# Kernel optimization log

Measured on AMD Instinct MI355X. Metric: run time of the kernel, lower is better.

## Reference

```python
import jax, jax.numpy as jnp
import numpy as np

L_LAYERS = 6
D = 768
H = 12
DH = D // H
FF = 3072
B = 32
LX = 256
LY = 128
EPS = 1e-6
NEG = -1e9


def setup_inputs() -> dict:
    key = jax.random.key(0)
    ks = jax.random.split(key, 24)
    s = 0.02
    f32 = jnp.float32
    inp = {
        'y': jax.random.normal(ks[0], (B, LY, D), f32),
        'x': jax.random.normal(ks[1], (B, LX, D), f32),
        'y_mask': jnp.zeros((B, 1, 1, LY), bool),
        'x_mask': jnp.zeros((B, 1, 1, LX), bool),
        'y_pos': jnp.arange(B * LY, dtype=jnp.int32).reshape(B, LY),
        'bbox': jax.random.normal(ks[2], (B, LX, 4), f32),
        # encoder (SA) params, stacked over layers; attn weight order: q,k,v,merge
        'enc_attn_w': jax.random.normal(ks[3], (L_LAYERS, 4, D, D), f32) * s,
        'enc_attn_b': jnp.zeros((L_LAYERS, 4, D), f32),
        'enc_ffn_w1': jax.random.normal(ks[4], (L_LAYERS, D, FF), f32) * s,
        'enc_ffn_b1': jnp.zeros((L_LAYERS, FF), f32),
        'enc_ffn_w2': jax.random.normal(ks[5], (L_LAYERS, FF, D), f32) * s,
        'enc_ffn_b2': jnp.zeros((L_LAYERS, D), f32),
        'enc_ln_g': jnp.ones((L_LAYERS, 2, D), f32),
        'enc_ln_b': jnp.zeros((L_LAYERS, 2, D), f32),
        # decoder (RELAGA) params; two attentions per layer (self, cross)
        'dec_attn_w': jax.random.normal(ks[6], (L_LAYERS, 2, 4, D, D), f32) * s,
        'dec_attn_b': jnp.zeros((L_LAYERS, 2, 4, D), f32),
        'dec_ffn_w1': jax.random.normal(ks[7], (L_LAYERS, D, FF), f32) * s,
        'dec_ffn_b1': jnp.zeros((L_LAYERS, FF), f32),
        'dec_ffn_w2': jax.random.normal(ks[8], (L_LAYERS, FF, D), f32) * s,
        'dec_ffn_b2': jnp.zeros((L_LAYERS, D), f32),
        'dec_ln_g': jnp.ones((L_LAYERS, 3, D), f32),
        'dec_ln_b': jnp.zeros((L_LAYERS, 3, D), f32),
    }
    return inp


def _layernorm(t, g, b):
    m = jnp.mean(t, axis=-1, keepdims=True)
    v = jnp.mean((t - m) ** 2, axis=-1, keepdims=True)
    return g * (t - m) / jnp.sqrt(v + EPS) + b


def _heads(t, w, bias):
    # [B,L,D] -> [B,H,L,DH]
    nb = t.shape[0]
    return (t @ w + bias).reshape(nb, -1, H, DH).transpose(0, 2, 1, 3)


def _mha(v, k, q, mask, w, bias, rel=None):
    # w: [4,D,D] (q,k,v,merge), bias: [4,D]; rel: [B,1,Lq,Lq] or None
    qh = _heads(q, w[0], bias[0])
    kh = _heads(k, w[1], bias[1])
    vh = _heads(v, w[2], bias[2])
    scores = jnp.einsum('bhqd,bhkd->bhqk', qh, kh) / np.sqrt(DH).astype(np.float32)
    scores = jnp.where(mask, NEG, scores)
    att = jax.nn.softmax(scores, axis=-1)
    out = jnp.einsum('bhqk,bhkd->bhqd', att, vh)
    if rel is not None:
        out = jnp.einsum('bhqp,bhpd->bhqd', rel, out)  # bbox-relational matmul
    nb = q.shape[0]
    out = out.transpose(0, 2, 1, 3).reshape(nb, -1, D)
    return out @ w[3] + bias[3]


def _ffn(t, w1, b1, w2, b2):
    return jnp.maximum(t @ w1 + b1, 0.0) @ w2 + b2


def reference(y, x, y_mask, x_mask, y_pos, bbox,
              enc_attn_w, enc_attn_b, enc_ffn_w1, enc_ffn_b1, enc_ffn_w2, enc_ffn_b2,
              enc_ln_g, enc_ln_b,
              dec_attn_w, dec_attn_b, dec_ffn_w1, dec_ffn_b1, dec_ffn_w2, dec_ffn_b2,
              dec_ln_g, dec_ln_b):
    # bbox cosine-similarity relation matrix (softmax over last dim), shared across heads
    prod = jnp.einsum('bic,bjc->bij', bbox, bbox)
    n = jnp.sqrt(jnp.sum(bbox * bbox, axis=-1))          # [B,LX]
    denom = n[:, :, None] * n[:, None, :]                 # [B,LX,LX]
    sim = jax.nn.softmax(prod / denom, axis=2)[:, None]   # [B,1,LX,LX] broadcasts over heads

    for i in range(L_LAYERS):  # encoder: SA stack over y
        att = _mha(y, y, y, y_mask, enc_attn_w[i], enc_attn_b[i])
        y = _layernorm(y + att, enc_ln_g[i, 0], enc_ln_b[i, 0])
        f = _ffn(y, enc_ffn_w1[i], enc_ffn_b1[i], enc_ffn_w2[i], enc_ffn_b2[i])
        y = _layernorm(y + f, enc_ln_g[i, 1], enc_ln_b[i, 1])

    for i in range(L_LAYERS):  # decoder: RELAGA stack over x
        att = _mha(x, x, x, x_mask, dec_attn_w[i, 0], dec_attn_b[i, 0], rel=sim)
        x = _layernorm(x + att, dec_ln_g[i, 0], dec_ln_b[i, 0])
        att = _mha(y, y, x, y_mask, dec_attn_w[i, 1], dec_attn_b[i, 1], rel=sim)
        x = _layernorm(x + att, dec_ln_g[i, 1], dec_ln_b[i, 1])
        f = _ffn(x, dec_ffn_w1[i], dec_ffn_b1[i], dec_ffn_w2[i], dec_ffn_b2[i])
        x = _layernorm(x + f, dec_ln_g[i, 2], dec_ln_b[i, 2])

    return (y, x)
```

## Files before the change

kernel.cpp:

```cpp
#include <hip/hip_runtime.h>

#define DEV __device__ __forceinline__

constexpr int NB  = 32;
constexpr int LXc = 256;
constexpr int LYc = 128;
constexpr int Dc  = 768;
constexpr int NH  = 12;
constexpr int FFc = 3072;

typedef unsigned short u16;
typedef float f32x4 __attribute__((ext_vector_type(4)));
typedef short s16x8 __attribute__((ext_vector_type(8)));

DEV u16 f2bf(float f) {
  unsigned u = __float_as_uint(f);
  u += 0x7FFFu + ((u >> 16) & 1u);
  return (u16)(u >> 16);
}
DEV float bf2f(u16 w) { return __uint_as_float(((unsigned)w) << 16); }
DEV float ldf(const void* p, long long i, int isbf) {
  return isbf ? bf2f(((const u16*)p)[i]) : ((const float*)p)[i];
}

DEV void gload16(const void* g, void* l) {
  __builtin_amdgcn_global_load_lds(
      (const __attribute__((address_space(1))) void*)g,
      (__attribute__((address_space(3))) void*)l, 16, 0, 0);
}
DEV void barx() {
  asm volatile("" ::: "memory");
  __builtin_amdgcn_s_barrier();
  asm volatile("" ::: "memory");
}

__global__ void k_detect(const u16* y, int* flag) {
  if (threadIdx.x == 0) {
    int cnt = 0;
    for (int i = 0; i < 256; ++i) {
      u16 w = y[i];
      int e = (w >> 7) & 0xFF;
      if (e == 0 || (e >= 112 && e <= 140)) cnt++;
    }
    *flag = (cnt >= 200) ? 1 : 0;
  }
}

__global__ void k_ingest_b(const void* src, u16* dst, long long n, const int* flag) {
  int isbf = *flag;
  long long i = (long long)blockIdx.x * blockDim.x + threadIdx.x;
  long long st = (long long)gridDim.x * blockDim.x;
  for (; i < n; i += st) dst[i] = isbf ? ((const u16*)src)[i] : f2bf(((const float*)src)[i]);
}

__global__ void k_cvt(const void* src, float* dst, long long n, const int* flag) {
  int isbf = *flag;
  long long i = (long long)blockIdx.x * blockDim.x + threadIdx.x;
  long long st = (long long)gridDim.x * blockDim.x;
  for (; i < n; i += st) dst[i] = ldf(src, i, isbf);
}

__global__ void k_emit(const u16* ybuf, const u16* xbuf, void* out,
                       const int* flag, long long ny, long long nt) {
  int isbf = *flag;
  long long i = (long long)blockIdx.x * blockDim.x + threadIdx.x;
  long long st = (long long)gridDim.x * blockDim.x;
  for (; i < nt; i += st) {
    u16 v = (i < ny) ? ybuf[i] : xbuf[i - ny];
    if (isbf) ((u16*)out)[i] = v;
    else      ((float*)out)[i] = bf2f(v);
  }
}

__global__ __launch_bounds__(256) void k_wt(const void* src, u16* dst, int R, int C, const int* flag) {
  int isbf = *flag;
  __shared__ u16 t[32][33];
  long long base = (long long)blockIdx.z * R * C;
  int c0 = blockIdx.x * 32, r0 = blockIdx.y * 32;
  int tx = threadIdx.x & 31, ty = threadIdx.x >> 5;
#pragma unroll
  for (int k = 0; k < 4; ++k) {
    int r = r0 + ty + k * 8;
    t[ty + k * 8][tx] = f2bf(ldf(src, base + (long long)r * C + (c0 + tx), isbf));
  }
  __syncthreads();
#pragma unroll
  for (int k = 0; k < 4; ++k) {
    int c = c0 + ty + k * 8;
    dst[base + (long long)c * R + (r0 + tx)] = t[tx][ty + k * 8];
  }
}

__global__ __launch_bounds__(256) void k_bboxsim(const void* bbox, const int* flag, u16* sim) {
  int isbf = *flag;
  int b = blockIdx.x >> 8, i = blockIdx.x & 255;
  int j = threadIdx.x;
  long long base = (long long)b * LXc * 4;
  float a[4], c[4];
#pragma unroll
  for (int t = 0; t < 4; ++t) {
    a[t] = ldf(bbox, base + (long long)i * 4 + t, isbf);
    c[t] = ldf(bbox, base + (long long)j * 4 + t, isbf);
  }
  float dot = a[0]*c[0] + a[1]*c[1] + a[2]*c[2] + a[3]*c[3];
  float na  = sqrtf(a[0]*a[0] + a[1]*a[1] + a[2]*a[2] + a[3]*a[3]);
  float ncn = sqrtf(c[0]*c[0] + c[1]*c[1] + c[2]*c[2] + c[3]*c[3]);
  float v = dot / (na * ncn);
  __shared__ float r1[4], r2[4];
  float m = v;
  for (int o = 32; o; o >>= 1) m = fmaxf(m, __shfl_xor(m, o));
  if ((threadIdx.x & 63) == 0) r1[threadIdx.x >> 6] = m;
  __syncthreads();
  m = fmaxf(fmaxf(r1[0], r1[1]), fmaxf(r1[2], r1[3]));
  float e = __expf(v - m);
  float s = e;
  for (int o = 32; o; o >>= 1) s += __shfl_xor(s, o);
  if ((threadIdx.x & 63) == 0) r2[threadIdx.x >> 6] = s;
  __syncthreads();
  s = r2[0] + r2[1] + r2[2] + r2[3];
  sim[((long long)b * LXc + i) * LXc + j] = f2bf(e / s);
}

__global__ __launch_bounds__(256) void k_lnres3(u16* curb, const u16* delta,
                                                const void* g, long long gOff,
                                                const void* bb, long long bOff,
                                                const int* flag) {
  int isbf = *flag;
  long long row = blockIdx.x;
  u16* xr = curb + row * Dc;
  const u16* dr = delta + row * Dc;
  int t = threadIdx.x;
  float v[3];
  float s = 0.f;
#pragma unroll
  for (int i = 0; i < 3; ++i) { int c = t + i * 256; v[i] = bf2f(xr[c]) + bf2f(dr[c]); s += v[i]; }
  __shared__ float r1[4], r2[4];
  for (int o = 32; o; o >>= 1) s += __shfl_xor(s, o);
  if ((t & 63) == 0) r1[t >> 6] = s;
  __syncthreads();
  float mean = (r1[0] + r1[1] + r1[2] + r1[3]) * (1.0f / 768.0f);
  float s2 = 0.f;
#pragma unroll
  for (int i = 0; i < 3; ++i) { float d = v[i] - mean; s2 += d * d; }
  for (int o = 32; o; o >>= 1) s2 += __shfl_xor(s2, o);
  if ((t & 63) == 0) r2[t >> 6] = s2;
  __syncthreads();
  float var = (r2[0] + r2[1] + r2[2] + r2[3]) * (1.0f / 768.0f);
  float rstd = rsqrtf(var + 1e-6f);
#pragma unroll
  for (int i = 0; i < 3; ++i) {
    int c = t + i * 256;
    float o = ldf(g, gOff + c, isbf) * (v[i] - mean) * rstd + ldf(bb, bOff + c, isbf);
    xr[c] = f2bf(o);
  }
}

template<int DEC>
__global__ __launch_bounds__(256) void k_attn(const u16* __restrict__ Q,
                                              const u16* __restrict__ Kb,
                                              const u16* __restrict__ Vt,
                                              u16* __restrict__ Out,
                                              int Lq, int Lk) {
  __shared__ __align__(16) u16 Kl[64 * 64];
  __shared__ __align__(16) u16 Vl[64 * 64];
  __shared__ __align__(16) u16 Pl[4][16][72];
  const int tid = threadIdx.x, wid = tid >> 6, lane = tid & 63;
  const int qt = blockIdx.x, h = blockIdx.y, b = blockIdx.z;
  const int q0 = qt * 64 + wid * 16;
  const int rl = lane & 15, sx = lane >> 4;
  const int srow = lane >> 3;
  const int scol8 = ((lane & 7) ^ srow) << 3;

  s16x8 qa[2];
  {
    const u16* qrow = Q + ((long long)b * Lq + q0 + rl) * Dc + h * 64;
    qa[0] = *(const s16x8*)(qrow + sx * 8);
    qa[1] = *(const s16x8*)(qrow + 32 + sx * 8);
  }
  f32x4 o[4] = {};
  float m[4], l[4];
#pragma unroll
  for (int e = 0; e < 4; ++e) { m[e] = -3.0e38f; l[e] = 0.f; }

  const long long kbase = (long long)b * Lk * Dc + h * 64;
  const long long vbase = ((long long)b * Dc + h * 64) * Lk;

  for (int k0 = 0; k0 < Lk; k0 += 64) {
#pragma unroll
    for (int g = 0; g < 2; ++g) {
      int chunk = g * 4 + wid;
      gload16(Kb + kbase + (long long)(k0 + chunk * 8 + srow) * Dc + scol8,
              (char*)Kl + chunk * 1024);
    }
#pragma unroll
    for (int g = 0; g < 2; ++g) {
      int chunk = g * 4 + wid;
      gload16(Vt + vbase + (long long)(chunk * 8 + srow) * Lk + k0 + scol8,
              (char*)Vl + chunk * 1024);
    }
    asm volatile("s_waitcnt vmcnt(0)" ::: "memory");
    barx();

    f32x4 s[4];
#pragma unroll
    for (int n = 0; n < 4; ++n) {
      s16x8 b0 = *(const s16x8*)((char*)Kl + (n * 16 + rl) * 128 + ((sx    ) ^ (rl & 7)) * 16);
      s16x8 b1 = *(const s16x8*)((char*)Kl + (n * 16 + rl) * 128 + ((sx + 4) ^ (rl & 7)) * 16);
      f32x4 acc = {};
      acc = __builtin_amdgcn_mfma_f32_16x16x32_bf16(qa[0], b0, acc, 0, 0, 0);
      acc = __builtin_amdgcn_mfma_f32_16x16x32_bf16(qa[1], b1, acc, 0, 0, 0);
      s[n] = acc;
    }
#pragma unroll
    for (int n = 0; n < 4; ++n)
#pragma unroll
      for (int e = 0; e < 4; ++e) s[n][e] *= 0.125f;

#pragma unroll
    for (int e = 0; e < 4; ++e) {
      float v = fmaxf(fmaxf(s[0][e], s[1][e]), fmaxf(s[2][e], s[3][e]));
      v = fmaxf(v, __shfl_xor(v, 1));
      v = fmaxf(v, __shfl_xor(v, 2));
      v = fmaxf(v, __shfl_xor(v, 4));
      v = fmaxf(v, __shfl_xor(v, 8));
      float mn = fmaxf(m[e], v);
      float alpha = __expf(m[e] - mn);
      m[e] = mn;
      float ls = 0.f;
#pragma unroll
      for (int n = 0; n < 4; ++n) {
        float p = __expf(s[n][e] - mn);
        s[n][e] = p;
        ls += p;
      }
      ls += __shfl_xor(ls, 1);
      ls += __shfl_xor(ls, 2);
      ls += __shfl_xor(ls, 4);
      ls += __shfl_xor(ls, 8);
      l[e] = l[e] * alpha + ls;
#pragma unroll
      for (int n = 0; n < 4; ++n) o[n][e] *= alpha;
    }

#pragma unroll
    for (int e = 0; e < 4; ++e)
#pragma unroll
      for (int n = 0; n < 4; ++n)
        Pl[wid][sx * 4 + e][n * 16 + rl] = f2bf(s[n][e]);
    barx();

    s16x8 pa0 = *(const s16x8*)&Pl[wid][rl][sx * 8];
    s16x8 pa1 = *(const s16x8*)&Pl[wid][rl][32 + sx * 8];
#pragma unroll
    for (int n = 0; n < 4; ++n) {
      s16x8 v0 = *(const s16x8*)((char*)Vl + (n * 16 + rl) * 128 + ((sx    ) ^ (rl & 7)) * 16);
      s16x8 v1 = *(const s16x8*)((char*)Vl + (n * 16 + rl) * 128 + ((sx + 4) ^ (rl & 7)) * 16);
      o[n] = __builtin_amdgcn_mfma_f32_16x16x32_bf16(pa0, v0, o[n], 0, 0, 0);
      o[n] = __builtin_amdgcn_mfma_f32_16x16x32_bf16(pa1, v1, o[n], 0, 0, 0);
    }
    barx();
  }

#pragma unroll
  for (int e = 0; e < 4; ++e) l[e] = 1.0f / l[e];
  if (DEC) {
    u16* Op = Out + ((long long)b * Dc + h * 64) * LXc;
#pragma unroll
    for (int n = 0; n < 4; ++n) {
      union { u16 u[4]; uint2 d; } pk;
#pragma unroll
      for (int e = 0; e < 4; ++e) pk.u[e] = f2bf(o[n][e] * l[e]);
      *(uint2*)&Op[(long long)(n * 16 + rl) * LXc + q0 + sx * 4] = pk.d;
    }
  } else {
    u16* Op = Out + ((long long)b * Lq + q0) * Dc + h * 64;
#pragma unroll
    for (int n = 0; n < 4; ++n)
#pragma unroll
      for (int e = 0; e < 4; ++e)
        Op[(long long)(sx * 4 + e) * Dc + n * 16 + rl] = f2bf(o[n][e] * l[e]);
  }
}

struct G2 {
  const u16* A; long long lda, sAb, sAh;
  const u16* W; long long ldw, sWb, sWh;
  const float* bias; long long bOff;
  void* C; long long ldc, sCb, sCh;
  void* Ck; void* Cv; int vSeg;
  int Hdim; float scale; int relu; int Lseq;
};

template<int BM, int BN, int MODE>
__global__ __launch_bounds__(256, 2) void gemm2(G2 p, int M, int N, int K) {
  constexpr int BK = 64;
  __shared__ __align__(16) u16 Al[BM * BK];
  __shared__ __align__(16) u16 Bl[BN * BK];
  const int tid = threadIdx.x, wid = tid >> 6, lane = tid & 63;
  const int z = blockIdx.z, zb = z / p.Hdim, zh = z % p.Hdim;
  int bx = blockIdx.x, by = blockIdx.y;
  if (gridDim.z == 1) {
    int gx = gridDim.x, nwg = gx * gridDim.y;
    int orig = by * gx + bx;
    int q = nwg >> 3, r = nwg & 7, xcd = orig & 7, lin = orig >> 3;
    int wg = (xcd < r ? xcd * (q + 1) : r * (q + 1) + (xcd - r) * q) + lin;
    bx = wg % gx; by = wg / gx;
  }
  const u16* A = p.A + (long long)zb * p.sAb + (long long)zh * p.sAh;
  const u16* W = p.W + (long long)zb * p.sWb + (long long)zh * p.sWh;
  const int m0 = by * BM, n0 = bx * BN;
  const int wr = wid >> 1, wc = wid & 1;
  constexpr int FM = BM / 32, FN = BN / 32;
  f32x4 acc[FM][FN] = {};
  const int lr = lane >> 3;
  const int lo = (((lane & 7) ^ lr) << 3) * 2;
  const int rl = lane & 15;
  const int sx = lane >> 4;
  const int slotb0 = (((sx + 0) ^ (rl & 7)) << 4);
  const int slotb1 = (((sx + 4) ^ (rl & 7)) << 4);

  for (int k0 = 0; k0 < K; k0 += BK) {
#pragma unroll
    for (int i = 0; i < BM / 32; ++i) {
      int chunk = wid * (BM / 32) + i;
      int row = chunk * 8 + lr;
      gload16((const char*)(A + (long long)(m0 + row) * p.lda + k0) + lo,
              (char*)Al + chunk * 1024);
    }
#pragma unroll
    for (int i = 0; i < BN / 32; ++i) {
      int chunk = wid * (BN / 32) + i;
      int row = chunk * 8 + lr;
      gload16((const char*)(W + (long long)(n0 + row) * p.ldw + k0) + lo,
              (char*)Bl + chunk * 1024);
    }
    __syncthreads();
    {
      s16x8 af[FM][2], bfr[FN][2];
#pragma unroll
      for (int i = 0; i < FM; ++i) {
        const char* rbase = (char*)Al + (wr * (BM / 2) + i * 16 + rl) * 128;
        af[i][0] = *(const s16x8*)(rbase + slotb0);
        af[i][1] = *(const s16x8*)(rbase + slotb1);
      }
#pragma unroll
      for (int j = 0; j < FN; ++j) {
        const char* rbase = (char*)Bl + (wc * (BN / 2) + j * 16 + rl) * 128;
        bfr[j][0] = *(const s16x8*)(rbase + slotb0);
        bfr[j][1] = *(const s16x8*)(rbase + slotb1);
      }
#pragma unroll
      for (int ks = 0; ks < 2; ++ks)
#pragma unroll
        for (int i = 0; i < FM; ++i)
#pragma unroll
          for (int j = 0; j < FN; ++j)
            acc[i][j] = __builtin_amdgcn_mfma_f32_16x16x32_bf16(af[i][ks], bfr[j][ks], acc[i][j], 0, 0, 0);
    }
    __syncthreads();
  }

  const int seg = (MODE == 4) ? (n0 / 768) : 0;
#pragma unroll
  for (int j = 0; j < FN; ++j) {
    int col = n0 + wc * (BN / 2) + j * 16 + (lane & 15);
    float bv = p.bias ? p.bias[p.bOff + col] : 0.f;
#pragma unroll
    for (int i = 0; i < FM; ++i) {
      int row0 = m0 + wr * (BM / 2) + i * 16 + (lane >> 4) * 4;
      if (MODE == 0) {
        u16* C = (u16*)p.C + (long long)zb * p.sCb + (long long)zh * p.sCh;
#pragma unroll
        for (int e = 0; e < 4; ++e) {
          float v = acc[i][j][e] * p.scale + bv;
          if (p.relu) v = fmaxf(v, 0.f);
          C[(long long)(row0 + e) * p.ldc + col] = f2bf(v);
        }
      } else {
        u16* outp = seg == 0 ? (u16*)p.C : (seg == 1 ? (u16*)p.Ck : (u16*)p.Cv);
        int c = col - seg * 768;
        if (seg == p.vSeg) {
          int b = row0 / p.Lseq, l = row0 % p.Lseq;
          union { u16 u[4]; uint2 d; } pk;
#pragma unroll
          for (int e = 0; e < 4; ++e) pk.u[e] = f2bf(acc[i][j][e] + bv);
          *(uint2*)&outp[((long long)b * Dc + c) * p.Lseq + l] = pk.d;
        } else {
#pragma unroll
          for (int e = 0; e < 4; ++e)
            outp[(long long)(row0 + e) * 768 + c] = f2bf(acc[i][j][e] + bv);
        }
      }
    }
  }
}

template<int BM, int BN, int MODE>
static void run_gemm(const G2& p, int M, int N, int K, int nz, hipStream_t st) {
  dim3 grid(N / BN, M / BM, nz);
  gemm2<BM, BN, MODE><<<grid, 256, 0, st>>>(p, M, N, K);
}

extern "C" void kernel_launch(void* const* d_in, const int* in_sizes, int n_in,
                              void* d_out, int out_size, void* d_ws, size_t ws_size,
                              hipStream_t stream) {
  const void* y_in  = d_in[0];
  const void* x_in  = d_in[1];
  const void* bbox  = d_in[5];
  const void* enc_aw = d_in[6];  const void* enc_ab = d_in[7];
  const void* enc_w1 = d_in[8];  const void* enc_b1 = d_in[9];
  const void* enc_w2 = d_in[10]; const void* enc_b2 = d_in[11];
  const void* enc_lg = d_in[12]; const void* enc_lb = d_in[13];
  const void* dec_aw = d_in[14]; const void* dec_ab = d_in[15];
  const void* dec_w1 = d_in[16]; const void* dec_b1 = d_in[17];
  const void* dec_w2 = d_in[18]; const void* dec_b2 = d_in[19];
  const void* dec_lg = d_in[20]; const void* dec_lb = d_in[21];

  char* base = (char*)d_ws;
  size_t off = 0;
  auto alloc = [&](size_t bytes) { void* p = base + off; off = (off + bytes + 255) & ~(size_t)255; return p; };
  int*  flag = (int*)alloc(256);
  const long long DD = (long long)Dc * Dc;
  const long long DF = (long long)Dc * FFc;
  u16* WencA  = (u16*)alloc(24 * DD * 2);
  u16* WencW1 = (u16*)alloc(6 * DF * 2);
  u16* WencW2 = (u16*)alloc(6 * DF * 2);
  u16* WdecA  = (u16*)alloc(48 * DD * 2);
  u16* WdecW1 = (u16*)alloc(6 * DF * 2);
  u16* WdecW2 = (u16*)alloc(6 * DF * 2);
  float* BencA  = (float*)alloc(24 * Dc * 4);
  float* BencW1 = (float*)alloc(6 * FFc * 4);
  float* BencW2 = (float*)alloc(6 * Dc * 4);
  float* BdecA  = (float*)alloc(48 * Dc * 4);
  float* BdecW1 = (float*)alloc(6 * FFc * 4);
  float* BdecW2 = (float*)alloc(6 * Dc * 4);
  const long long NYt = (long long)NB * LYc * Dc;
  const long long NXt = (long long)NB * LXc * Dc;
  u16*   curb_y = (u16*)alloc(NYt * 2);
  u16*   curb_x = (u16*)alloc(NXt * 2);
  u16*   simb   = (u16*)alloc((long long)NB * LXc * LXc * 2);
  u16*   qbf    = (u16*)alloc(NXt * 2);
  u16*   kbf    = (u16*)alloc(NXt * 2);
  u16*   vT     = (u16*)alloc(NXt * 2);
  u16*   deltab = (u16*)alloc(NXt * 2);
  u16*   aoT    = (u16*)alloc(NXt * 2);
  u16*   ao2    = (u16*)alloc(NXt * 2);
  u16*   ffmid  = (u16*)alloc((long long)NB * LXc * FFc * 2);

  k_detect<<<1, 64, 0, stream>>>((const u16*)y_in, flag);
  k_ingest_b<<<1024, 256, 0, stream>>>(y_in, curb_y, NYt, flag);
  k_ingest_b<<<1024, 256, 0, stream>>>(x_in, curb_x, NXt, flag);
  k_bboxsim<<<NB * LXc, 256, 0, stream>>>(bbox, flag, simb);
  k_wt<<<dim3(Dc/32, Dc/32, 24), 256, 0, stream>>>(enc_aw, WencA, Dc, Dc, flag);
  k_wt<<<dim3(FFc/32, Dc/32, 6), 256, 0, stream>>>(enc_w1, WencW1, Dc, FFc, flag);
  k_wt<<<dim3(Dc/32, FFc/32, 6), 256, 0, stream>>>(enc_w2, WencW2, FFc, Dc, flag);
  k_wt<<<dim3(Dc/32, Dc/32, 48), 256, 0, stream>>>(dec_aw, WdecA, Dc, Dc, flag);
  k_wt<<<dim3(FFc/32, Dc/32, 6), 256, 0, stream>>>(dec_w1, WdecW1, Dc, FFc, flag);
  k_wt<<<dim3(Dc/32, FFc/32, 6), 256, 0, stream>>>(dec_w2, WdecW2, FFc, Dc, flag);
  k_cvt<<<32, 256, 0, stream>>>(enc_ab, BencA, 24 * Dc, flag);
  k_cvt<<<32, 256, 0, stream>>>(enc_b1, BencW1, 6 * FFc, flag);
  k_cvt<<<32, 256, 0, stream>>>(enc_b2, BencW2, 6 * Dc, flag);
  k_cvt<<<32, 256, 0, stream>>>(dec_ab, BdecA, 48 * Dc, flag);
  k_cvt<<<32, 256, 0, stream>>>(dec_b1, BdecW1, 6 * FFc, flag);
  k_cvt<<<32, 256, 0, stream>>>(dec_b2, BdecW2, 6 * Dc, flag);

  auto qkv = [&](const u16* A, int M, const u16* Wt, long long wOff,
                 const float* bias, long long bOff, int Lseq) {
    G2 p{}; p.A = A; p.lda = Dc; p.W = Wt + wOff; p.ldw = Dc;
    p.bias = bias; p.bOff = bOff;
    p.C = qbf; p.Ck = kbf; p.Cv = vT; p.vSeg = 2;
    p.Hdim = 1; p.scale = 1.f; p.Lseq = Lseq;
    run_gemm<128, 128, 4>(p, M, 3 * Dc, Dc, 1, stream);
  };
  auto kv = [&](const u16* A, int M, const u16* Wt, long long wOff,
                const float* bias, long long bOff, int Lseq) {
    G2 p{}; p.A = A; p.lda = Dc; p.W = Wt + wOff; p.ldw = Dc;
    p.bias = bias; p.bOff = bOff;
    p.C = kbf; p.Ck = vT; p.vSeg = 1;
    p.Hdim = 1; p.scale = 1.f; p.Lseq = Lseq;
    run_gemm<128, 128, 4>(p, M, 2 * Dc, Dc, 1, stream);
  };
  auto p768 = [&](const u16* A, int M, const u16* Wt, long long wOff,
                  const float* bias, long long bOff, u16* C, int K, int relu) {
    G2 p{}; p.A = A; p.lda = K; p.W = Wt + wOff; p.ldw = K;
    p.bias = bias; p.bOff = bOff; p.C = C; p.ldc = Dc;
    p.Hdim = 1; p.scale = 1.f; p.relu = relu;
    run_gemm<128, 64, 0>(p, M, Dc, K, 1, stream);
  };
  auto ffn1 = [&](const u16* A, int M, const u16* Wt, long long wOff,
                  const float* bias, long long bOff) {
    G2 p{}; p.A = A; p.lda = Dc; p.W = Wt + wOff; p.ldw = Dc;
    p.bias = bias; p.bOff = bOff; p.C = ffmid; p.ldc = FFc;
    p.Hdim = 1; p.scale = 1.f; p.relu = 1;
    run_gemm<128, 128, 0>(p, M, FFc, Dc, 1, stream);
  };
  auto g_rel = [&]() {
    G2 p{}; p.A = simb; p.lda = LXc; p.sAb = (long long)LXc * LXc;
    p.W = aoT; p.ldw = LXc; p.sWb = (long long)Dc * LXc;
    p.C = ao2; p.ldc = Dc; p.sCb = (long long)LXc * Dc;
    p.Hdim = 1; p.scale = 1.f;
    run_gemm<128, 128, 0>(p, LXc, Dc, LXc, NB, stream);
  };

  for (int i = 0; i < 6; ++i) {
    int M = NB * LYc;
    long long wo = (long long)i * 4 * DD, bo = (long long)i * 4 * Dc;
    qkv(curb_y, M, WencA, wo, BencA, bo, LYc);
    k_attn<0><<<dim3(LYc / 64, NH, NB), 256, 0, stream>>>(qbf, kbf, vT, ao2, LYc, LYc);
    p768(ao2, M, WencA, wo + 3 * DD, BencA, bo + 3 * Dc, deltab, Dc, 0);
    k_lnres3<<<M, 256, 0, stream>>>(curb_y, deltab, enc_lg, (long long)(i*2+0)*Dc, enc_lb, (long long)(i*2+0)*Dc, flag);
    ffn1(curb_y, M, WencW1, (long long)i * DF, BencW1, (long long)i * FFc);
    p768(ffmid, M, WencW2, (long long)i * DF, BencW2, (long long)i * Dc, deltab, FFc, 0);
    k_lnres3<<<M, 256, 0, stream>>>(curb_y, deltab, enc_lg, (long long)(i*2+1)*Dc, enc_lb, (long long)(i*2+1)*Dc, flag);
  }

  for (int i = 0; i < 6; ++i) {
    int M = NB * LXc;
    for (int a = 0; a < 2; ++a) {
      long long wo = (long long)(i * 2 + a) * 4 * DD;
      long long bo = (long long)(i * 2 + a) * 4 * Dc;
      int Lk;
      if (a == 0) {
        qkv(curb_x, M, WdecA, wo, BdecA, bo, LXc);
        Lk = LXc;
      } else {
        p768(curb_x, M, WdecA, wo, BdecA, bo, qbf, Dc, 0);
        kv(curb_y, NB * LYc, WdecA, wo + DD, BdecA, bo + Dc, LYc);
        Lk = LYc;
      }
      k_attn<1><<<dim3(LXc / 64, NH, NB), 256, 0, stream>>>(qbf, kbf, vT, aoT, LXc, Lk);
      g_rel();
      p768(ao2, M, WdecA, wo + 3 * DD, BdecA, bo + 3 * Dc, deltab, Dc, 0);
      k_lnres3<<<M, 256, 0, stream>>>(curb_x, deltab, dec_lg, (long long)(i*3+a)*Dc, dec_lb, (long long)(i*3+a)*Dc, flag);
    }
    ffn1(curb_x, M, WdecW1, (long long)i * DF, BdecW1, (long long)i * FFc);
    p768(ffmid, M, WdecW2, (long long)i * DF, BdecW2, (long long)i * Dc, deltab, FFc, 0);
    k_lnres3<<<M, 256, 0, stream>>>(curb_x, deltab, dec_lg, (long long)(i*3+2)*Dc, dec_lb, (long long)(i*3+2)*Dc, flag);
  }

  k_emit<<<2048, 256, 0, stream>>>(curb_y, curb_x, d_out, flag, NYt, NYt + NXt);
}
```

Measured before the change: 3.167 ms.

## Double-buffer GEMM LDS tiles and vectorize residual layernorm loads

```diff
diff --git a/kernel.cpp b/kernel.cpp
--- a/kernel.cpp
+++ b/kernel.cpp
@@ -121,7 +121,7 @@
   sim[((long long)b * LXc + i) * LXc + j] = f2bf(e / s);
 }
 
-__global__ __launch_bounds__(256) void k_lnres3(u16* curb, const u16* delta,
+__global__ __launch_bounds__(192) void k_lnres4(u16* curb, const u16* delta,
                                                 const void* g, long long gOff,
                                                 const void* bb, long long bOff,
                                                 const int* flag) {
@@ -130,29 +130,34 @@
   u16* xr = curb + row * Dc;
   const u16* dr = delta + row * Dc;
   int t = threadIdx.x;
-  float v[3];
+  union { u16 u[4]; uint2 d; } xa, da;
+  xa.d = *(const uint2*)(xr + t * 4);
+  da.d = *(const uint2*)(dr + t * 4);
+  float v[4];
   float s = 0.f;
 #pragma unroll
-  for (int i = 0; i < 3; ++i) { int c = t + i * 256; v[i] = bf2f(xr[c]) + bf2f(dr[c]); s += v[i]; }
-  __shared__ float r1[4], r2[4];
+  for (int i = 0; i < 4; ++i) { v[i] = bf2f(xa.u[i]) + bf2f(da.u[i]); s += v[i]; }
+  __shared__ float r1[3], r2[3];
   for (int o = 32; o; o >>= 1) s += __shfl_xor(s, o);
   if ((t & 63) == 0) r1[t >> 6] = s;
   __syncthreads();
-  float mean = (r1[0] + r1[1] + r1[2] + r1[3]) * (1.0f / 768.0f);
+  float mean = (r1[0] + r1[1] + r1[2]) * (1.0f / 768.0f);
   float s2 = 0.f;
 #pragma unroll
-  for (int i = 0; i < 3; ++i) { float d = v[i] - mean; s2 += d * d; }
+  for (int i = 0; i < 4; ++i) { float d = v[i] - mean; s2 += d * d; }
   for (int o = 32; o; o >>= 1) s2 += __shfl_xor(s2, o);
   if ((t & 63) == 0) r2[t >> 6] = s2;
   __syncthreads();
-  float var = (r2[0] + r2[1] + r2[2] + r2[3]) * (1.0f / 768.0f);
+  float var = (r2[0] + r2[1] + r2[2]) * (1.0f / 768.0f);
   float rstd = rsqrtf(var + 1e-6f);
-#pragma unroll
-  for (int i = 0; i < 3; ++i) {
-    int c = t + i * 256;
+  union { u16 u[4]; uint2 d; } oa;
+#pragma unroll
+  for (int i = 0; i < 4; ++i) {
+    int c = t * 4 + i;
     float o = ldf(g, gOff + c, isbf) * (v[i] - mean) * rstd + ldf(bb, bOff + c, isbf);
-    xr[c] = f2bf(o);
-  }
+    oa.u[i] = f2bf(o);
+  }
+  *(uint2*)(xr + t * 4) = oa.d;
 }
 
 template<int DEC>
@@ -294,8 +299,9 @@
 template<int BM, int BN, int MODE>
 __global__ __launch_bounds__(256, 2) void gemm2(G2 p, int M, int N, int K) {
   constexpr int BK = 64;
-  __shared__ __align__(16) u16 Al[BM * BK];
-  __shared__ __align__(16) u16 Bl[BN * BK];
+  constexpr int NLD = BM / 32 + BN / 32;
+  __shared__ __align__(16) u16 Al[2][BM * BK];
+  __shared__ __align__(16) u16 Bl[2][BN * BK];
   const int tid = threadIdx.x, wid = tid >> 6, lane = tid & 63;
   const int z = blockIdx.z, zb = z / p.Hdim, zh = z % p.Hdim;
   int bx = blockIdx.x, by = blockIdx.y;
@@ -319,33 +325,48 @@
   const int slotb0 = (((sx + 0) ^ (rl & 7)) << 4);
   const int slotb1 = (((sx + 4) ^ (rl & 7)) << 4);
 
-  for (int k0 = 0; k0 < K; k0 += BK) {
-#pragma unroll
-    for (int i = 0; i < BM / 32; ++i) {
-      int chunk = wid * (BM / 32) + i;
+  auto stage = [&](int t, int bb) {
+    long long k0 = (long long)t * BK;
+#pragma unroll
+    for (int i = 0; i < FM; ++i) {
+      int chunk = wid * FM + i;
       int row = chunk * 8 + lr;
       gload16((const char*)(A + (long long)(m0 + row) * p.lda + k0) + lo,
-              (char*)Al + chunk * 1024);
-    }
-#pragma unroll
-    for (int i = 0; i < BN / 32; ++i) {
-      int chunk = wid * (BN / 32) + i;
+              (char*)Al[bb] + chunk * 1024);
+    }
+#pragma unroll
+    for (int i = 0; i < FN; ++i) {
+      int chunk = wid * FN + i;
       int row = chunk * 8 + lr;
       gload16((const char*)(W + (long long)(n0 + row) * p.ldw + k0) + lo,
-              (char*)Bl + chunk * 1024);
-    }
-    __syncthreads();
+              (char*)Bl[bb] + chunk * 1024);
+    }
+  };
+
+  const int NT = K / BK;
+  stage(0, 0);
+  for (int t = 0; t < NT; ++t) {
+    const int bb = t & 1;
+    if (t + 1 < NT) {
+      stage(t + 1, bb ^ 1);
+      if constexpr (NLD == 8)      asm volatile("s_waitcnt vmcnt(8)" ::: "memory");
+      else if constexpr (NLD == 6) asm volatile("s_waitcnt vmcnt(6)" ::: "memory");
+      else                         asm volatile("s_waitcnt vmcnt(0)" ::: "memory");
+    } else {
+      asm volatile("s_waitcnt vmcnt(0)" ::: "memory");
+    }
+    barx();
     {
       s16x8 af[FM][2], bfr[FN][2];
 #pragma unroll
       for (int i = 0; i < FM; ++i) {
-        const char* rbase = (char*)Al + (wr * (BM / 2) + i * 16 + rl) * 128;
+        const char* rbase = (char*)Al[bb] + (wr * (BM / 2) + i * 16 + rl) * 128;
         af[i][0] = *(const s16x8*)(rbase + slotb0);
         af[i][1] = *(const s16x8*)(rbase + slotb1);
       }
 #pragma unroll
       for (int j = 0; j < FN; ++j) {
-        const char* rbase = (char*)Bl + (wc * (BN / 2) + j * 16 + rl) * 128;
+        const char* rbase = (char*)Bl[bb] + (wc * (BN / 2) + j * 16 + rl) * 128;
         bfr[j][0] = *(const s16x8*)(rbase + slotb0);
         bfr[j][1] = *(const s16x8*)(rbase + slotb1);
       }
@@ -357,7 +378,7 @@
           for (int j = 0; j < FN; ++j)
             acc[i][j] = __builtin_amdgcn_mfma_f32_16x16x32_bf16(af[i][ks], bfr[j][ks], acc[i][j], 0, 0, 0);
     }
-    __syncthreads();
+    barx();
   }
 
   const int seg = (MODE == 4) ? (n0 / 768) : 0;
@@ -508,10 +529,10 @@
     qkv(curb_y, M, WencA, wo, BencA, bo, LYc);
     k_attn<0><<<dim3(LYc / 64, NH, NB), 256, 0, stream>>>(qbf, kbf, vT, ao2, LYc, LYc);
     p768(ao2, M, WencA, wo + 3 * DD, BencA, bo + 3 * Dc, deltab, Dc, 0);
-    k_lnres3<<<M, 256, 0, stream>>>(curb_y, deltab, enc_lg, (long long)(i*2+0)*Dc, enc_lb, (long long)(i*2+0)*Dc, flag);
+    k_lnres4<<<M, 192, 0, stream>>>(curb_y, deltab, enc_lg, (long long)(i*2+0)*Dc, enc_lb, (long long)(i*2+0)*Dc, flag);
     ffn1(curb_y, M, WencW1, (long long)i * DF, BencW1, (long long)i * FFc);
     p768(ffmid, M, WencW2, (long long)i * DF, BencW2, (long long)i * Dc, deltab, FFc, 0);
-    k_lnres3<<<M, 256, 0, stream>>>(curb_y, deltab, enc_lg, (long long)(i*2+1)*Dc, enc_lb, (long long)(i*2+1)*Dc, flag);
+    k_lnres4<<<M, 192, 0, stream>>>(curb_y, deltab, enc_lg, (long long)(i*2+1)*Dc, enc_lb, (long long)(i*2+1)*Dc, flag);
   }
 
   for (int i = 0; i < 6; ++i) {
@@ -531,11 +552,11 @@
       k_attn<1><<<dim3(LXc / 64, NH, NB), 256, 0, stream>>>(qbf, kbf, vT, aoT, LXc, Lk);
       g_rel();
       p768(ao2, M, WdecA, wo + 3 * DD, BdecA, bo + 3 * Dc, deltab, Dc, 0);
-      k_lnres3<<<M, 256, 0, stream>>>(curb_x, deltab, dec_lg, (long long)(i*3+a)*Dc, dec_lb, (long long)(i*3+a)*Dc, flag);
+      k_lnres4<<<M, 192, 0, stream>>>(curb_x, deltab, dec_lg, (long long)(i*3+a)*Dc, dec_lb, (long long)(i*3+a)*Dc, flag);
     }
     ffn1(curb_x, M, WdecW1, (long long)i * DF, BdecW1, (long long)i * FFc);
     p768(ffmid, M, WdecW2, (long long)i * DF, BdecW2, (long long)i * Dc, deltab, FFc, 0);
-    k_lnres3<<<M, 256, 0, stream>>>(curb_x, deltab, dec_lg, (long long)(i*3+2)*Dc, dec_lb, (long long)(i*3+2)*Dc, flag);
+    k_lnres4<<<M, 192, 0, stream>>>(curb_x, deltab, dec_lg, (long long)(i*3+2)*Dc, dec_lb, (long long)(i*3+2)*Dc, flag);
   }
 
   k_emit<<<2048, 256, 0, stream>>>(curb_y, curb_x, d_out, flag, NYt, NYt + NXt);
```

Measured after the change: 3.436 ms. 8.5% more time.
